# Performance work log

Hardware: AMD Instinct MI355X
Metric: run time of the kernel (lower is better)

The kernel has to match this reference:

```python
import jax, jax.numpy as jnp
import numpy as np
from jax import lax


def _lstm_layer(x, W_ih, W_hh, b_ih, b_hh):
    """Single LSTM layer, batch_first x: [B, T, in] -> (out [B,T,H], h_n [B,H], c_n [B,H]).
    PyTorch gate order: i, f, g, o."""
    B, T, _ = x.shape
    H = W_hh.shape[1]
    # Precompute input contributions for all timesteps (one big GEMM).
    xg = jnp.einsum('bti,gi->btg', x, W_ih) + b_ih + b_hh  # [B, T, 4H]
    h0 = jnp.zeros((B, H), dtype=x.dtype)
    c0 = jnp.zeros((B, H), dtype=x.dtype)

    def step(carry, g_t):
        h, c = carry
        gates = g_t + h @ W_hh.T  # [B, 4H]
        i, f, g, o = jnp.split(gates, 4, axis=-1)
        i = jax.nn.sigmoid(i)
        f = jax.nn.sigmoid(f)
        g = jnp.tanh(g)
        o = jax.nn.sigmoid(o)
        c = f * c + i * g
        h = o * jnp.tanh(c)
        return (h, c), h

    (h_n, c_n), hs = lax.scan(step, (h0, c0), jnp.swapaxes(xg, 0, 1))  # hs: [T, B, H]
    return jnp.swapaxes(hs, 0, 1), h_n, c_n


def setup_inputs() -> dict:
    key = jax.random.key(0)
    ks = jax.random.split(key, 12)
    H = 128
    IN = 1
    B, T = 256, 2048
    s = 1.0 / np.sqrt(H)  # PyTorch default init scale

    def u(k, shape):
        return jax.random.uniform(k, shape, jnp.float32, -s, s)

    return {
        'x': jax.random.normal(ks[0], (B, T, IN), jnp.float32),
        'W_ih_l0': u(ks[1], (4 * H, IN)),
        'W_hh_l0': u(ks[2], (4 * H, H)),
        'b_ih_l0': u(ks[3], (4 * H,)),
        'b_hh_l0': u(ks[4], (4 * H,)),
        'W_ih_l1': u(ks[5], (4 * H, H)),
        'W_hh_l1': u(ks[6], (4 * H, H)),
        'b_ih_l1': u(ks[7], (4 * H,)),
        'b_hh_l1': u(ks[8], (4 * H,)),
        'W_fc': u(ks[9], (1, H)),
        'b_fc': u(ks[10], (1,)),
    }


def reference(x, W_ih_l0, W_hh_l0, b_ih_l0, b_hh_l0,
              W_ih_l1, W_hh_l1, b_ih_l1, b_hh_l1, W_fc, b_fc):
    out0, h0, c0 = _lstm_layer(x, W_ih_l0, W_hh_l0, b_ih_l0, b_hh_l0)
    out1, h1, c1 = _lstm_layer(out0, W_ih_l1, W_hh_l1, b_ih_l1, b_hh_l1)
    last = out1[:, -1, :]                 # [B, H]
    y = last @ W_fc.T + b_fc              # [B, 1]
    h_n = jnp.stack([h0, h1], axis=0)     # [num_layers, B, H]
    c_n = jnp.stack([c0, c1], axis=0)
    return (y, h_n, c_n)
```

## Files before the change

kernel.cpp:

```cpp
#include <hip/hip_runtime.h>

#define T_SEQ 2048
#define HDIM  128
#define GDIM  512
#define BATCH 256

typedef _Float16 f16;
typedef _Float16 f16x2 __attribute__((ext_vector_type(2)));
typedef _Float16 f16x8 __attribute__((ext_vector_type(8)));

#if __has_builtin(__builtin_amdgcn_fdot2)
__device__ __forceinline__ float dot2(f16x2 a, f16x2 b, float c) {
    return __builtin_amdgcn_fdot2(a, b, c, false);
}
#else
__device__ __forceinline__ float dot2(f16x2 a, f16x2 b, float c) {
    return c + (float)a[0] * (float)b[0] + (float)a[1] * (float)b[1];
}
#endif

__device__ __forceinline__ f16x2 mk2(float a, float b) {
    f16x2 r; r[0] = (f16)a; r[1] = (f16)b; return r;
}
__device__ __forceinline__ f16x2 pr(f16x8 v, int m) {
    f16x2 r; r[0] = v[2 * m]; r[1] = v[2 * m + 1]; return r;
}

__device__ __forceinline__ float sigm(float x) {
    return __builtin_amdgcn_rcpf(1.0f + __expf(-x));
}
__device__ __forceinline__ float tanh_fast(float x) {
    float e = __expf(2.0f * x);
    return 1.0f - 2.0f * __builtin_amdgcn_rcpf(e + 1.0f);
}

__global__ __launch_bounds__(512, 2)
void lstm_fused(const float* __restrict__ x,
                const float* __restrict__ Wih0,
                const float* __restrict__ Whh0,
                const float* __restrict__ bih0,
                const float* __restrict__ bhh0,
                const float* __restrict__ Wih1,
                const float* __restrict__ Whh1,
                const float* __restrict__ bih1,
                const float* __restrict__ bhh1,
                const float* __restrict__ Wfc,
                const float* __restrict__ bfc,
                float* __restrict__ out)
{
    __shared__ __align__(16) f16   wh1s[GDIM * 72];
    __shared__ __align__(16) float xs[T_SEQ];
    __shared__ __align__(16) f16   h0h[HDIM];
    __shared__ __align__(16) f16   h1h[HDIM];
    __shared__ float h0f[HDIM], h1f[HDIM];
    __shared__ float g0[GDIM], g1[GDIM];

    const int t = threadIdx.x;
    const int b = blockIdx.x;

    ((float4*)xs)[t] = ((const float4*)(x + (size_t)b * T_SEQ))[t];

    f16x2 w0[64];
    f16x2 wi[64];
    f16x2 wl[32];
    {
        const float4* p0 = (const float4*)(Whh0 + t * HDIM);
        const float4* p1 = (const float4*)(Wih1 + t * HDIM);
        const float4* p2 = (const float4*)(Whh1 + t * HDIM);
#pragma unroll
        for (int c = 0; c < 32; ++c) {
            float4 v = p0[c];
            w0[2 * c]     = mk2(v.x, v.y);
            w0[2 * c + 1] = mk2(v.z, v.w);
        }
#pragma unroll
        for (int c = 0; c < 32; ++c) {
            float4 v = p1[c];
            wi[2 * c]     = mk2(v.x, v.y);
            wi[2 * c + 1] = mk2(v.z, v.w);
        }
#pragma unroll
        for (int c = 0; c < 16; ++c) {
            float4 v = p2[c];
            wl[2 * c]     = mk2(v.x, v.y);
            wl[2 * c + 1] = mk2(v.z, v.w);
        }
        f16x2* dst = (f16x2*)(wh1s + t * 72);
#pragma unroll
        for (int c = 0; c < 16; ++c) {
            float4 v = p2[16 + c];
            dst[2 * c]     = mk2(v.x, v.y);
            dst[2 * c + 1] = mk2(v.z, v.w);
        }
    }
    const float wx0   = Wih0[t];
    const float bias0 = bih0[t] + bhh0[t];
    const float bias1 = bih1[t] + bhh1[t];

    if (t < HDIM) {
        h0h[t] = (f16)0.f; h1h[t] = (f16)0.f;
        h0f[t] = 0.f;      h1f[t] = 0.f;
    }
    float c0r = 0.f, c1r = 0.f;
    __syncthreads();

    const f16x8* h0p  = (const f16x8*)h0h;
    const f16x8* h1p  = (const f16x8*)h1h;
    const f16x8* wrow = (const f16x8*)(wh1s + t * 72);

    for (int i = 0; i <= T_SEQ; ++i) {
        float a0 = (i < T_SEQ ? xs[i] : 0.f) * wx0 + bias0;
        float a1 = bias1;
#pragma unroll
        for (int c = 0; c < 16; ++c) {
            f16x8 h = h0p[c];
#pragma unroll
            for (int m = 0; m < 4; ++m) {
                f16x2 hp = pr(h, m);
                a0 = dot2(w0[4 * c + m], hp, a0);
                a1 = dot2(wi[4 * c + m], hp, a1);
            }
        }
#pragma unroll
        for (int c = 0; c < 8; ++c) {
            f16x8 h = h1p[c];
#pragma unroll
            for (int m = 0; m < 4; ++m)
                a1 = dot2(wl[4 * c + m], pr(h, m), a1);
        }
#pragma unroll
        for (int c = 0; c < 8; ++c) {
            f16x8 h = h1p[8 + c];
            f16x8 w = wrow[c];
#pragma unroll
            for (int m = 0; m < 4; ++m)
                a1 = dot2(pr(w, m), pr(h, m), a1);
        }
        g0[t] = a0;
        g1[t] = a1;
        __syncthreads();

        if (t < 128) {
            if (i < T_SEQ) {
                float gi = sigm(g0[t]);
                float gf = sigm(g0[t + 128]);
                float gg = tanh_fast(g0[t + 256]);
                float go = sigm(g0[t + 384]);
                c0r = gf * c0r + gi * gg;
                float h = go * tanh_fast(c0r);
                h0h[t] = (f16)h;
                h0f[t] = h;
            }
        } else if (t < 256) {
            if (i >= 1) {
                int j = t - 128;
                float gi = sigm(g1[j]);
                float gf = sigm(g1[j + 128]);
                float gg = tanh_fast(g1[j + 256]);
                float go = sigm(g1[j + 384]);
                c1r = gf * c1r + gi * gg;
                float h = go * tanh_fast(c1r);
                h1h[j] = (f16)h;
                h1f[j] = h;
            }
        }
        __syncthreads();
    }

    float* hn = out + BATCH;
    float* cn = out + BATCH + 2 * BATCH * HDIM;
    if (t < 128) {
        hn[(size_t)b * HDIM + t] = h0f[t];
        cn[(size_t)b * HDIM + t] = c0r;
    } else if (t < 256) {
        int j = t - 128;
        hn[BATCH * HDIM + (size_t)b * HDIM + j] = h1f[j];
        cn[BATCH * HDIM + (size_t)b * HDIM + j] = c1r;
    }
    if (t < 64) {
        float p = h1f[t] * Wfc[t] + h1f[t + 64] * Wfc[t + 64];
#pragma unroll
        for (int o = 32; o >= 1; o >>= 1) p += __shfl_down(p, o);
        if (t == 0) out[b] = p + bfc[0];
    }
}

extern "C" void kernel_launch(void* const* d_in, const int* in_sizes, int n_in,
                              void* d_out, int out_size, void* d_ws, size_t ws_size,
                              hipStream_t stream) {
    const float* x    = (const float*)d_in[0];
    const float* Wih0 = (const float*)d_in[1];
    const float* Whh0 = (const float*)d_in[2];
    const float* bih0 = (const float*)d_in[3];
    const float* bhh0 = (const float*)d_in[4];
    const float* Wih1 = (const float*)d_in[5];
    const float* Whh1 = (const float*)d_in[6];
    const float* bih1 = (const float*)d_in[7];
    const float* bhh1 = (const float*)d_in[8];
    const float* Wfc  = (const float*)d_in[9];
    const float* bfc  = (const float*)d_in[10];
    lstm_fused<<<BATCH, 512, 0, stream>>>(x, Wih0, Whh0, bih0, bhh0,
                                          Wih1, Whh1, bih1, bhh1,
                                          Wfc, bfc, (float*)d_out);
}
```

Measured before the change: 2.638 ms.

## Split gate dot products across 1024 threads with register-only weights

Each block now runs 1024 threads: the first 512 compute the layer-0 recurrent gates plus half of the layer-1 recurrent product, and the second 512 compute the layer-1 input product plus the other half. The shared-memory copy of W_hh1 is dropped because all weights now fit in registers. Each dot product uses two interleaved accumulators to shorten dependency chains. The layer-1 gate sum gains one extra shared-memory add, and doubling the threads per block raises block-wide barrier cost and per-CU register pressure.

```diff
diff --git a/kernel.cpp b/kernel.cpp
--- a/kernel.cpp
+++ b/kernel.cpp
@@ -34,7 +34,7 @@
     return 1.0f - 2.0f * __builtin_amdgcn_rcpf(e + 1.0f);
 }
 
-__global__ __launch_bounds__(512, 2)
+__global__ __launch_bounds__(1024)
 void lstm_fused(const float* __restrict__ x,
                 const float* __restrict__ Wih0,
                 const float* __restrict__ Whh0,
@@ -48,54 +48,41 @@
                 const float* __restrict__ bfc,
                 float* __restrict__ out)
 {
-    __shared__ __align__(16) f16   wh1s[GDIM * 72];
     __shared__ __align__(16) float xs[T_SEQ];
     __shared__ __align__(16) f16   h0h[HDIM];
     __shared__ __align__(16) f16   h1h[HDIM];
     __shared__ float h0f[HDIM], h1f[HDIM];
-    __shared__ float g0[GDIM], g1[GDIM];
+    __shared__ float g0[GDIM];
+    __shared__ float g1a[GDIM], g1b[GDIM];
 
-    const int t = threadIdx.x;
-    const int b = blockIdx.x;
+    const int t  = threadIdx.x;
+    const int b  = blockIdx.x;
+    const bool gA = (t < 512);
+    const int r  = t & 511;
 
-    ((float4*)xs)[t] = ((const float4*)(x + (size_t)b * T_SEQ))[t];
+    if (gA)
+        ((float4*)xs)[t] = ((const float4*)(x + (size_t)b * T_SEQ))[t];
 
-    f16x2 w0[64];
-    f16x2 wi[64];
-    f16x2 wl[32];
+    f16x2 wa[64];
+    f16x2 wb[32];
     {
-        const float4* p0 = (const float4*)(Whh0 + t * HDIM);
-        const float4* p1 = (const float4*)(Wih1 + t * HDIM);
-        const float4* p2 = (const float4*)(Whh1 + t * HDIM);
+        const float4* pa = (const float4*)((gA ? Whh0 : Wih1) + r * HDIM);
+        const float4* pb = (const float4*)(Whh1 + r * HDIM + (gA ? 0 : 64));
 #pragma unroll
         for (int c = 0; c < 32; ++c) {
-            float4 v = p0[c];
-            w0[2 * c]     = mk2(v.x, v.y);
-            w0[2 * c + 1] = mk2(v.z, v.w);
-        }
-#pragma unroll
-        for (int c = 0; c < 32; ++c) {
-            float4 v = p1[c];
-            wi[2 * c]     = mk2(v.x, v.y);
-            wi[2 * c + 1] = mk2(v.z, v.w);
+            float4 v = pa[c];
+            wa[2 * c]     = mk2(v.x, v.y);
+            wa[2 * c + 1] = mk2(v.z, v.w);
         }
 #pragma unroll
         for (int c = 0; c < 16; ++c) {
-            float4 v = p2[c];
-            wl[2 * c]     = mk2(v.x, v.y);
-            wl[2 * c + 1] = mk2(v.z, v.w);
-        }
-        f16x2* dst = (f16x2*)(wh1s + t * 72);
-#pragma unroll
-        for (int c = 0; c < 16; ++c) {
-            float4 v = p2[16 + c];
-            dst[2 * c]     = mk2(v.x, v.y);
-            dst[2 * c + 1] = mk2(v.z, v.w);
+            float4 v = pb[c];
+            wb[2 * c]     = mk2(v.x, v.y);
+            wb[2 * c + 1] = mk2(v.z, v.w);
         }
     }
-    const float wx0   = Wih0[t];
-    const float bias0 = bih0[t] + bhh0[t];
-    const float bias1 = bih1[t] + bhh1[t];
+    const float xw   = gA ? Wih0[r] : 0.f;
+    const float bias = gA ? (bih0[r] + bhh0[r]) : (bih1[r] + bhh1[r]);
 
     if (t < HDIM) {
         h0h[t] = (f16)0.f; h1h[t] = (f16)0.f;
@@ -105,39 +92,33 @@
     __syncthreads();
 
     const f16x8* h0p  = (const f16x8*)h0h;
-    const f16x8* h1p  = (const f16x8*)h1h;
-    const f16x8* wrow = (const f16x8*)(wh1s + t * 72);
+    const f16x8* hsel = ((const f16x8*)h1h) + (gA ? 0 : 8);
 
     for (int i = 0; i <= T_SEQ; ++i) {
-        float a0 = (i < T_SEQ ? xs[i] : 0.f) * wx0 + bias0;
-        float a1 = bias1;
+        float sa = (i < T_SEQ ? xs[i] : 0.f) * xw + bias;
+        float sb = 0.f, sc = 0.f, sd = 0.f;
 #pragma unroll
         for (int c = 0; c < 16; ++c) {
             f16x8 h = h0p[c];
-#pragma unroll
-            for (int m = 0; m < 4; ++m) {
-                f16x2 hp = pr(h, m);
-                a0 = dot2(w0[4 * c + m], hp, a0);
-                a1 = dot2(wi[4 * c + m], hp, a1);
-            }
+            sa = dot2(wa[4 * c + 0], pr(h, 0), sa);
+            sb = dot2(wa[4 * c + 1], pr(h, 1), sb);
+            sa = dot2(wa[4 * c + 2], pr(h, 2), sa);
+            sb = dot2(wa[4 * c + 3], pr(h, 3), sb);
         }
 #pragma unroll
         for (int c = 0; c < 8; ++c) {
-            f16x8 h = h1p[c];
-#pragma unroll
-            for (int m = 0; m < 4; ++m)
-                a1 = dot2(wl[4 * c + m], pr(h, m), a1);
+            f16x8 h = hsel[c];
+            sc = dot2(wb[4 * c + 0], pr(h, 0), sc);
+            sd = dot2(wb[4 * c + 1], pr(h, 1), sd);
+            sc = dot2(wb[4 * c + 2], pr(h, 2), sc);
+            sd = dot2(wb[4 * c + 3], pr(h, 3), sd);
         }
-#pragma unroll
-        for (int c = 0; c < 8; ++c) {
-            f16x8 h = h1p[8 + c];
-            f16x8 w = wrow[c];
-#pragma unroll
-            for (int m = 0; m < 4; ++m)
-                a1 = dot2(pr(w, m), pr(h, m), a1);
+        if (gA) {
+            g0[r]  = sa + sb;
+            g1a[r] = sc + sd;
+        } else {
+            g1b[r] = (sa + sb) + (sc + sd);
         }
-        g0[t] = a0;
-        g1[t] = a1;
         __syncthreads();
 
         if (t < 128) {
@@ -151,13 +132,13 @@
                 h0h[t] = (f16)h;
                 h0f[t] = h;
             }
-        } else if (t < 256) {
+        } else if (t >= 512 && t < 640) {
             if (i >= 1) {
-                int j = t - 128;
-                float gi = sigm(g1[j]);
-                float gf = sigm(g1[j + 128]);
-                float gg = tanh_fast(g1[j + 256]);
-                float go = sigm(g1[j + 384]);
+                int j = t - 512;
+                float gi = sigm(g1a[j]       + g1b[j]);
+                float gf = sigm(g1a[j + 128] + g1b[j + 128]);
+                float gg = tanh_fast(g1a[j + 256] + g1b[j + 256]);
+                float go = sigm(g1a[j + 384] + g1b[j + 384]);
                 c1r = gf * c1r + gi * gg;
                 float h = go * tanh_fast(c1r);
                 h1h[j] = (f16)h;
@@ -172,8 +153,8 @@
     if (t < 128) {
         hn[(size_t)b * HDIM + t] = h0f[t];
         cn[(size_t)b * HDIM + t] = c0r;
-    } else if (t < 256) {
-        int j = t - 128;
+    } else if (t >= 512 && t < 640) {
+        int j = t - 512;
         hn[BATCH * HDIM + (size_t)b * HDIM + j] = h1f[j];
         cn[BATCH * HDIM + (size_t)b * HDIM + j] = c1r;
     }
@@ -199,7 +180,7 @@
     const float* bhh1 = (const float*)d_in[8];
     const float* Wfc  = (const float*)d_in[9];
     const float* bfc  = (const float*)d_in[10];
-    lstm_fused<<<BATCH, 512, 0, stream>>>(x, Wih0, Whh0, bih0, bhh0,
-                                          Wih1, Whh1, bih1, bhh1,
-                                          Wfc, bfc, (float*)d_out);
+    lstm_fused<<<BATCH, 1024, 0, stream>>>(x, Wih0, Whh0, bih0, bhh0,
+                                           Wih1, Whh1, bih1, bhh1,
+                                           Wfc, bfc, (float*)d_out);
 }
```

New measurement: 3.079 ms. +16.7%, slower.
